# Kernel tuning notes

Measured on AMD Instinct MI355X. Metric: run time of the kernel, lower is better.

## Reference

```python
import jax, jax.numpy as jnp
import numpy as np

D_MODEL = 1024
N_HEADS = 16
MAX_SEQ_LEN = 2048

def setup_inputs() -> dict:
    key = jax.random.key(0)
    ks = jax.random.split(key, 4)
    B, L, D = 2, 2048, D_MODEL
    s = 0.02
    x = jax.random.normal(ks[0], (B, L, D), dtype=jnp.float32)
    qkv_w = jax.random.normal(ks[1], (D, 3 * D), dtype=jnp.float32) * s
    qkv_b = jnp.zeros((3 * D,), dtype=jnp.float32)
    proj_w = jax.random.normal(ks[2], (D, D), dtype=jnp.float32) * s
    proj_b = jnp.zeros((D,), dtype=jnp.float32)
    bias_table = jax.random.normal(ks[3], (2 * MAX_SEQ_LEN - 1, N_HEADS), dtype=jnp.float32) * s
    return {"x": x, "qkv_w": qkv_w, "qkv_b": qkv_b, "proj_w": proj_w, "proj_b": proj_b, "bias_table": bias_table}

def reference(x, qkv_w, qkv_b, proj_w, proj_b, bias_table):
    B, L, D = x.shape
    H = N_HEADS
    dk = D // H
    scale = dk ** -0.5
    # fused qkv projection: (B,L,3,H,dk)
    qkv = (x @ qkv_w + qkv_b).reshape(B, L, 3, H, dk)
    q = qkv[:, :, 0].transpose(0, 2, 1, 3)  # (B,H,L,dk)
    k = qkv[:, :, 1].transpose(0, 2, 1, 3)
    v = qkv[:, :, 2].transpose(0, 2, 1, 3)
    attn = jnp.einsum("bhqd,bhkd->bhqk", q, k) * scale  # (B,H,L,L)
    # relative position bias gather (Swin-style)
    coords = jnp.arange(L)
    rel_idx = coords[None, :] - coords[:, None] + (MAX_SEQ_LEN - 1)  # (L,L)
    rel_bias = bias_table[rel_idx]  # (L,L,H)
    attn = attn + rel_bias.transpose(2, 0, 1)[None]  # (B,H,L,L)
    attn = jax.nn.softmax(attn, axis=-1)
    out = jnp.einsum("bhqk,bhkd->bhqd", attn, v)  # (B,H,L,dk)
    out = out.transpose(0, 2, 1, 3).reshape(B, L, D)
    return out @ proj_w + proj_b
```

## Files before the change

kernel.cpp:

```cpp
#include <hip/hip_runtime.h>
#include <stdint.h>

typedef __attribute__((ext_vector_type(4))) float    f32x4;
typedef __attribute__((ext_vector_type(8))) short    bf16x8;
typedef __attribute__((ext_vector_type(2))) uint32_t u32x2;

#define MFMA16(a,b,c) __builtin_amdgcn_mfma_f32_16x16x32_bf16((a),(b),(c),0,0,0)

__device__ __forceinline__ uint16_t f2bf(float f){
  uint32_t u = __float_as_uint(f);
  return (uint16_t)((u + 0x7FFFu + ((u >> 16) & 1u)) >> 16);
}

__device__ __forceinline__ uint32_t pk_bf16(float lo, float hi){
  uint32_t r; asm("v_cvt_pk_bf16_f32 %0, %1, %2" : "=v"(r) : "v"(lo), "v"(hi)); return r;
}

__device__ __forceinline__ float fast_exp2(float x){
  float r; asm("v_exp_f32 %0, %1" : "=v"(r) : "v"(x)); return r;
}

__device__ __forceinline__ void gload16(const uint16_t* g, uint16_t* l){
  __builtin_amdgcn_global_load_lds((const __attribute__((address_space(1))) uint32_t*)g,
                                   (__attribute__((address_space(3))) uint32_t*)l, 16, 0, 0);
}

__global__ void k_cvt(const float* __restrict__ in, uint16_t* __restrict__ out){
  const size_t i = (size_t)(blockIdx.x*256 + threadIdx.x) * 4;
  const f32x4 v = *(const f32x4*)(in + i);
  u32x2 pk = {pk_bf16(v[0], v[1]), pk_bf16(v[2], v[3])};
  *(u32x2*)(out + i) = pk;
}

__global__ void k_tcvt(const float* __restrict__ in, uint16_t* __restrict__ out, int K, int N){
  __shared__ float tile[64][65];
  const int k0 = blockIdx.y*64, n0 = blockIdx.x*64;
  const int tc = threadIdx.x & 63, tr = threadIdx.x >> 6;
  #pragma unroll
  for (int p=0;p<16;p++){ int r = p*4 + tr; tile[r][tc] = in[(size_t)(k0+r)*N + n0 + tc]; }
  __syncthreads();
  #pragma unroll
  for (int p=0;p<16;p++){ int r = p*4 + tr; out[(size_t)(n0+r)*K + k0 + tc] = f2bf(tile[tc][r]); }
}

__global__ void k_biast(const float* __restrict__ in, float* __restrict__ out){
  const int i = blockIdx.x*256 + threadIdx.x;
  if (i < 4095*16) out[(i & 15)*4096 + (i >> 4)] = in[i] * 1.4426950408889634f;
}

template<int EPI>
__global__ __launch_bounds__(256, 2) void k_gemm(
    const uint16_t* __restrict__ A, const uint16_t* __restrict__ Bt,
    const float* __restrict__ bias,
    uint16_t* __restrict__ qo, uint16_t* __restrict__ ko, uint16_t* __restrict__ vto,
    float* __restrict__ outf)
{
  __shared__ __align__(16) uint16_t at[128*64];
  __shared__ __align__(16) uint16_t bt[128*64];
  const int tid = threadIdx.x;
  const int lane = tid & 63, w = tid >> 6;
  const int g = lane >> 4, li = lane & 15;
  const int wr = w >> 1, wc = w & 1;
  const int m0 = blockIdx.y * 128, n0 = blockIdx.x * 128;

  f32x4 acc[4][4] = {};

  const int srow = tid >> 3;
  const int scg  = (tid & 7) ^ (srow & 7);

  for (int kt_ = 0; kt_ < 16; kt_++){
    const int kk = kt_*64;
    __syncthreads();
    #pragma unroll
    for (int j = 0; j < 4; j++){
      gload16(A  + (size_t)(m0 + j*32 + srow)*1024 + kk + scg*8, at + (j*256+tid)*8);
      gload16(Bt + (size_t)(n0 + j*32 + srow)*1024 + kk + scg*8, bt + (j*256+tid)*8);
    }
    asm volatile("s_waitcnt vmcnt(0)" ::: "memory");
    __syncthreads();

    bf16x8 af[2][4], bfr[2][4];
    #pragma unroll
    for (int mi=0; mi<4; mi++){
      int row = wr*64 + mi*16 + li, sw = row & 7;
      af[0][mi] = *(const bf16x8*)(at + row*64 + ((g     ^ sw)*8));
      af[1][mi] = *(const bf16x8*)(at + row*64 + (((4+g) ^ sw)*8));
    }
    #pragma unroll
    for (int ni=0; ni<4; ni++){
      int row = wc*64 + ni*16 + li, sw = row & 7;
      bfr[0][ni] = *(const bf16x8*)(bt + row*64 + ((g     ^ sw)*8));
      bfr[1][ni] = *(const bf16x8*)(bt + row*64 + (((4+g) ^ sw)*8));
    }
    #pragma unroll
    for (int s=0; s<2; s++)
      #pragma unroll
      for (int mi=0; mi<4; mi++)
        #pragma unroll
        for (int ni=0; ni<4; ni++)
          acc[mi][ni] = MFMA16(af[s][mi], bfr[s][ni], acc[mi][ni]);
  }

  if (EPI == 0){
    #pragma unroll
    for (int ni=0; ni<4; ni++){
      const int c = n0 + wc*64 + ni*16 + li;
      const float bv = bias[c];
      const int which = c >> 10, cc = c & 1023;
      const int h = cc >> 6, d = cc & 63;
      #pragma unroll
      for (int mi=0; mi<4; mi++){
        const int trow = m0 + wr*64 + mi*16 + g*4;
        const int b_ = trow >> 11, lcl = trow & 2047;
        const f32x4 v4 = acc[mi][ni];
        if (which == 0){
          uint16_t* dst = qo + (((size_t)(b_*16 + h)*2048 + lcl)*64 + d);
          #pragma unroll
          for (int r=0;r<4;r++) dst[(size_t)r*64] = f2bf((v4[r] + bv) * 0.18033688011112042f);
        } else if (which == 1){
          uint16_t* dst = ko + (((size_t)(b_*16 + h)*2048 + lcl)*64 + d);
          #pragma unroll
          for (int r=0;r<4;r++) dst[(size_t)r*64] = f2bf(v4[r] + bv);
        } else {
          u32x2 pk = {pk_bf16(v4[0]+bv, v4[1]+bv), pk_bf16(v4[2]+bv, v4[3]+bv)};
          *(u32x2*)(vto + (((size_t)(b_*16 + h)*64 + d)*2048 + lcl)) = pk;
        }
      }
    }
  } else {
    #pragma unroll
    for (int ni=0; ni<4; ni++){
      const int c = n0 + wc*64 + ni*16 + li;
      const float bv = bias[c];
      #pragma unroll
      for (int mi=0; mi<4; mi++){
        const int trow = m0 + wr*64 + mi*16 + g*4;
        float* dst = outf + (size_t)trow*1024 + c;
        const f32x4 v4 = acc[mi][ni];
        #pragma unroll
        for (int r=0;r<4;r++) dst[(size_t)r*1024] = v4[r] + bv;
      }
    }
  }
}

__global__ __launch_bounds__(512, 4) void k_attn(
    const uint16_t* __restrict__ qg, const uint16_t* __restrict__ kg,
    const uint16_t* __restrict__ vg, const float* __restrict__ biast,
    uint16_t* __restrict__ outp)
{
  __shared__ __align__(16) uint16_t kt[2][64*64];
  __shared__ __align__(16) uint16_t vt[2][64*64];
  __shared__ __align__(16) uint16_t pt[8][16*64];
  __shared__ float bl[2176];
  const int tid = threadIdx.x;
  const int lane = tid & 63, w = tid >> 6;
  const int g = lane >> 4, li = lane & 15;
  const int bh = blockIdx.y, h = bh & 15, b_ = bh >> 4;
  const int qb0 = blockIdx.x * 128;

  for (int i = tid; i < 2175; i += 512) bl[i] = biast[h*4096 + 1920 - qb0 + i];

  bf16x8 qf[2];
  {
    const uint16_t* qp = qg + ((size_t)bh*2048 + qb0 + w*16 + li)*64 + g*8;
    qf[0] = *(const bf16x8*)(qp);
    qf[1] = *(const bf16x8*)(qp + 32);
  }
  f32x4 o[4] = {};
  float mrun = -__builtin_inff(), lrun = 0.f;
  const uint16_t* kbase = kg + (size_t)bh*(2048*64);
  const uint16_t* vbase = vg + (size_t)bh*(64*2048);
  const int srow = tid >> 3;
  const int scg  = (tid & 7) ^ (srow & 7);
  const int q_l = w*16 + li;
  uint16_t* pl = &pt[w][0];
  const int swp = li & 7;

  __syncthreads();

  gload16(kbase + (size_t)srow*64        + scg*8, &kt[0][tid*8]);
  gload16(vbase + (size_t)srow*2048      + scg*8, &vt[0][tid*8]);

  for (int t = 0; t < 32; t++){
    const int cur = t & 1;
    if (t < 31){
      const int kv1 = (t+1)*64;
      gload16(kbase + (size_t)(kv1 + srow)*64  + scg*8, &kt[cur^1][tid*8]);
      gload16(vbase + (size_t)srow*2048 + kv1  + scg*8, &vt[cur^1][tid*8]);
      asm volatile("s_waitcnt vmcnt(2)" ::: "memory");
    } else {
      asm volatile("s_waitcnt vmcnt(0)" ::: "memory");
    }
    __builtin_amdgcn_s_barrier();
    const uint16_t* ktc = &kt[cur][0];
    const uint16_t* vtc = &vt[cur][0];
    const int kv0 = t*64;

    f32x4 sa[4];
    #pragma unroll
    for (int mf=0; mf<4; mf++){
      const int row = mf*16 + li, sw = row & 7;
      bf16x8 a0 = *(const bf16x8*)(ktc + row*64 + ((g     ^ sw)*8));
      bf16x8 a1 = *(const bf16x8*)(ktc + row*64 + (((4+g) ^ sw)*8));
      f32x4 cfr = {};
      cfr = MFMA16(a0, qf[0], cfr);
      cfr = MFMA16(a1, qf[1], cfr);
      sa[mf] = cfr;
    }

    const int ib0 = kv0 + g*4 + 127 - q_l;
    float tmax = -__builtin_inff();
    #pragma unroll
    for (int mf=0; mf<4; mf++){
      #pragma unroll
      for (int r=0; r<4; r++){
        float vv = sa[mf][r] + bl[ib0 + mf*16 + r];
        sa[mf][r] = vv;
        tmax = fmaxf(tmax, vv);
      }
    }
    tmax = fmaxf(tmax, __shfl_xor(tmax, 16));
    tmax = fmaxf(tmax, __shfl_xor(tmax, 32));
    const float mnew = fmaxf(mrun, tmax);
    const float alpha = fast_exp2(mrun - mnew);
    mrun = mnew;
    lrun *= alpha;
    #pragma unroll
    for (int i=0;i<4;i++) o[i] *= alpha;
    float psum = 0.f;
    #pragma unroll
    for (int mf=0; mf<4; mf++){
      float p0 = fast_exp2(sa[mf][0] - mnew);
      float p1 = fast_exp2(sa[mf][1] - mnew);
      float p2 = fast_exp2(sa[mf][2] - mnew);
      float p3 = fast_exp2(sa[mf][3] - mnew);
      psum += (p0+p1)+(p2+p3);
      const int ch = (2*mf + (g>>1)) ^ swp;
      u32x2 pk = {pk_bf16(p0,p1), pk_bf16(p2,p3)};
      *(u32x2*)(pl + li*64 + ch*8 + (g&1)*4) = pk;
    }
    psum += __shfl_xor(psum, 16);
    psum += __shfl_xor(psum, 32);
    lrun += psum;

    #pragma unroll
    for (int s=0; s<2; s++){
      bf16x8 pb = *(const bf16x8*)(pl + li*64 + (((4*s+g) ^ swp)*8));
      #pragma unroll
      for (int mf=0; mf<4; mf++){
        const int row = mf*16 + li, sw = row & 7;
        bf16x8 av = *(const bf16x8*)(vtc + row*64 + (((4*s+g) ^ sw)*8));
        o[mf] = MFMA16(av, pb, o[mf]);
      }
    }
    __builtin_amdgcn_s_barrier();
  }

  const float inv = 1.0f / lrun;
  const size_t token = (size_t)b_*2048 + qb0 + w*16 + li;
  #pragma unroll
  for (int mf=0; mf<4; mf++){
    u32x2 pk = {pk_bf16(o[mf][0]*inv, o[mf][1]*inv), pk_bf16(o[mf][2]*inv, o[mf][3]*inv)};
    *(u32x2*)(outp + token*1024 + h*64 + mf*16 + g*4) = pk;
  }
}

extern "C" void kernel_launch(void* const* d_in, const int* in_sizes, int n_in,
                              void* d_out, int out_size, void* d_ws, size_t ws_size,
                              hipStream_t stream)
{
  const float* x      = (const float*)d_in[0];
  const float* qkv_w  = (const float*)d_in[1];
  const float* qkv_b  = (const float*)d_in[2];
  const float* proj_w = (const float*)d_in[3];
  const float* proj_b = (const float*)d_in[4];
  const float* btab   = (const float*)d_in[5];
  float* out = (float*)d_out;

  char* p = (char*)d_ws;
  uint16_t* x_bf    = (uint16_t*)(p);
  uint16_t* qkv_wt  = (uint16_t*)(p + 8388608);
  uint16_t* proj_wt = (uint16_t*)(p + 14680064);
  uint16_t* q_buf   = (uint16_t*)(p + 16777216);
  uint16_t* k_buf   = (uint16_t*)(p + 25165824);
  uint16_t* vt_buf  = (uint16_t*)(p + 33554432);
  uint16_t* ao_buf  = (uint16_t*)(p + 41943040);
  float*    bias_t  = (float*)   (p + 50331648);

  k_cvt  <<<dim3(4096),  dim3(256), 0, stream>>>(x, x_bf);
  k_tcvt <<<dim3(48,16), dim3(256), 0, stream>>>(qkv_w,  qkv_wt,  1024, 3072);
  k_tcvt <<<dim3(16,16), dim3(256), 0, stream>>>(proj_w, proj_wt, 1024, 1024);
  k_biast<<<dim3(256),   dim3(256), 0, stream>>>(btab, bias_t);

  k_gemm<0><<<dim3(24,32), dim3(256), 0, stream>>>(x_bf, qkv_wt, qkv_b, q_buf, k_buf, vt_buf, nullptr);
  k_attn   <<<dim3(16,32), dim3(512), 0, stream>>>(q_buf, k_buf, vt_buf, bias_t, ao_buf);
  k_gemm<1><<<dim3(8,32),  dim3(256), 0, stream>>>(ao_buf, proj_wt, proj_b, nullptr, nullptr, nullptr, out);
}
```

Measured before the change: 137.5 us.

## Restructure attention: 32 queries per wave, lazy rescale, MFMA row sums

The attention kernel now runs 256 threads per block, with each wave handling two 16-query chunks, so every K/V fragment read from LDS feeds twice as many MFMAs. The row-sum reduction is replaced by an extra MFMA against a ones vector. Max rescaling is skipped when the new max is within a threshold of the running max. Bias values are prefetched from global memory into registers one tile ahead instead of being staged through shared memory. This cuts LDS traffic, shuffles and exp work per tile, but raises register pressure and lowers wave count per block.

```diff
diff --git a/kernel.cpp b/kernel.cpp
--- a/kernel.cpp
+++ b/kernel.cpp
@@ -144,125 +144,180 @@
   }
 }
 
-__global__ __launch_bounds__(512, 4) void k_attn(
+__device__ __forceinline__ void attn_tile(
+    int t, bool last, int tid, int g, int li, int srow, int scg,
+    const uint16_t* kbase, const uint16_t* vbase, const float* bb,
+    const uint16_t* ktc, uint16_t* ktn, const uint16_t* vtc, uint16_t* vtn, uint16_t* pl,
+    const bf16x8 (&qf)[2][2], bf16x8 ones,
+    f32x4 (&o)[4][2], f32x4 (&o4)[2], float& mrun0, float& mrun1,
+    const float (&bvC)[2][4][4], float (&bvN)[2][4][4])
+{
+  if (!last){
+    const int kv1 = (t+1)*64;
+    gload16(kbase + (size_t)(kv1+srow)*64 + scg*8,         ktn + tid*8);
+    gload16(kbase + (size_t)(kv1+srow+32)*64 + scg*8,      ktn + 2048 + tid*8);
+    gload16(vbase + (size_t)srow*2048 + kv1 + scg*8,       vtn + tid*8);
+    gload16(vbase + (size_t)(srow+32)*2048 + kv1 + scg*8,  vtn + 2048 + tid*8);
+    #pragma unroll
+    for (int c=0;c<2;c++)
+      #pragma unroll
+      for (int mf=0;mf<4;mf++)
+        #pragma unroll
+        for (int r=0;r<4;r++)
+          bvN[c][mf][r] = bb[kv1 + mf*16 + g*4 + r - c*16 - li];
+    asm volatile("s_waitcnt vmcnt(36)" ::: "memory");
+  } else {
+    asm volatile("s_waitcnt vmcnt(0)" ::: "memory");
+  }
+  __builtin_amdgcn_s_barrier();
+
+  f32x4 sa[4][2];
+  #pragma unroll
+  for (int mf=0; mf<4; mf++){
+    const int row = mf*16 + li, sw = row & 7;
+    bf16x8 a0 = *(const bf16x8*)(ktc + row*64 + ((g     ^ sw)*8));
+    bf16x8 a1 = *(const bf16x8*)(ktc + row*64 + (((4+g) ^ sw)*8));
+    #pragma unroll
+    for (int c=0;c<2;c++){
+      f32x4 cfr = {};
+      cfr = MFMA16(a0, qf[c][0], cfr);
+      cfr = MFMA16(a1, qf[c][1], cfr);
+      sa[mf][c] = cfr;
+    }
+  }
+
+  float t0 = -__builtin_inff(), t1 = -__builtin_inff();
+  #pragma unroll
+  for (int mf=0; mf<4; mf++){
+    #pragma unroll
+    for (int r=0; r<4; r++){
+      sa[mf][0][r] += bvC[0][mf][r];
+      sa[mf][1][r] += bvC[1][mf][r];
+    }
+    t0 = fmaxf(t0, fmaxf(fmaxf(sa[mf][0][0], sa[mf][0][1]), fmaxf(sa[mf][0][2], sa[mf][0][3])));
+    t1 = fmaxf(t1, fmaxf(fmaxf(sa[mf][1][0], sa[mf][1][1]), fmaxf(sa[mf][1][2], sa[mf][1][3])));
+  }
+  t0 = fmaxf(t0, __shfl_xor(t0, 16)); t0 = fmaxf(t0, __shfl_xor(t0, 32));
+  t1 = fmaxf(t1, __shfl_xor(t1, 16)); t1 = fmaxf(t1, __shfl_xor(t1, 32));
+
+  const int ok = (t0 <= mrun0 + 8.f) && (t1 <= mrun1 + 8.f);
+  if (!__all(ok)){
+    const float mn0 = fmaxf(mrun0, t0), mn1 = fmaxf(mrun1, t1);
+    const float a0 = fast_exp2(mrun0 - mn0), a1 = fast_exp2(mrun1 - mn1);
+    #pragma unroll
+    for (int mf=0; mf<4; mf++){ o[mf][0] *= a0; o[mf][1] *= a1; }
+    o4[0] *= a0; o4[1] *= a1;
+    mrun0 = mn0; mrun1 = mn1;
+  }
+
+  const int swp2 = 2*(li & 7);
+  #pragma unroll
+  for (int c=0;c<2;c++){
+    const float mr = c ? mrun1 : mrun0;
+    #pragma unroll
+    for (int mf=0; mf<4; mf++){
+      float p0 = fast_exp2(sa[mf][c][0] - mr);
+      float p1 = fast_exp2(sa[mf][c][1] - mr);
+      float p2 = fast_exp2(sa[mf][c][2] - mr);
+      float p3 = fast_exp2(sa[mf][c][3] - mr);
+      u32x2 pk = {pk_bf16(p0,p1), pk_bf16(p2,p3)};
+      *(u32x2*)(pl + (c*16+li)*64 + (((4*mf+g) ^ swp2)*4)) = pk;
+    }
+  }
+
+  bf16x8 av[2][4];
+  #pragma unroll
+  for (int s=0; s<2; s++)
+    #pragma unroll
+    for (int mf=0; mf<4; mf++){
+      const int row = mf*16 + li, sw = row & 7;
+      av[s][mf] = *(const bf16x8*)(vtc + row*64 + (((4*s+g) ^ sw)*8));
+    }
+  #pragma unroll
+  for (int c=0;c<2;c++){
+    #pragma unroll
+    for (int s=0; s<2; s++){
+      bf16x8 pb = *(const bf16x8*)(pl + (c*16+li)*64 + (((8*s+2*g) ^ swp2)*4));
+      o4[c] = MFMA16(ones, pb, o4[c]);
+      #pragma unroll
+      for (int mf=0; mf<4; mf++)
+        o[mf][c] = MFMA16(av[s][mf], pb, o[mf][c]);
+    }
+  }
+  __builtin_amdgcn_s_barrier();
+}
+
+__global__ __launch_bounds__(256, 2) void k_attn(
     const uint16_t* __restrict__ qg, const uint16_t* __restrict__ kg,
     const uint16_t* __restrict__ vg, const float* __restrict__ biast,
     uint16_t* __restrict__ outp)
 {
   __shared__ __align__(16) uint16_t kt[2][64*64];
   __shared__ __align__(16) uint16_t vt[2][64*64];
-  __shared__ __align__(16) uint16_t pt[8][16*64];
-  __shared__ float bl[2176];
+  __shared__ __align__(16) uint16_t pt[4][32*64];
   const int tid = threadIdx.x;
   const int lane = tid & 63, w = tid >> 6;
   const int g = lane >> 4, li = lane & 15;
   const int bh = blockIdx.y, h = bh & 15, b_ = bh >> 4;
   const int qb0 = blockIdx.x * 128;
-
-  for (int i = tid; i < 2175; i += 512) bl[i] = biast[h*4096 + 1920 - qb0 + i];
-
-  bf16x8 qf[2];
-  {
-    const uint16_t* qp = qg + ((size_t)bh*2048 + qb0 + w*16 + li)*64 + g*8;
-    qf[0] = *(const bf16x8*)(qp);
-    qf[1] = *(const bf16x8*)(qp + 32);
-  }
-  f32x4 o[4] = {};
-  float mrun = -__builtin_inff(), lrun = 0.f;
+  const int qw = qb0 + w*32;
+
+  bf16x8 qf[2][2];
+  #pragma unroll
+  for (int c=0;c<2;c++){
+    const uint16_t* qp = qg + ((size_t)bh*2048 + qw + c*16 + li)*64 + g*8;
+    qf[c][0] = *(const bf16x8*)(qp);
+    qf[c][1] = *(const bf16x8*)(qp + 32);
+  }
+  bf16x8 ones = (bf16x8)(short)0;
+  if (li == 0){ const short v = (short)0x3F80; ones = (bf16x8){v,v,v,v,v,v,v,v}; }
+
+  f32x4 o[4][2] = {};
+  f32x4 o4[2] = {};
+  float mrun0 = -__builtin_inff(), mrun1 = -__builtin_inff();
+
   const uint16_t* kbase = kg + (size_t)bh*(2048*64);
   const uint16_t* vbase = vg + (size_t)bh*(64*2048);
   const int srow = tid >> 3;
   const int scg  = (tid & 7) ^ (srow & 7);
-  const int q_l = w*16 + li;
+  const float* bb = biast + h*4096 + 2047 - qw;
   uint16_t* pl = &pt[w][0];
-  const int swp = li & 7;
-
-  __syncthreads();
-
-  gload16(kbase + (size_t)srow*64        + scg*8, &kt[0][tid*8]);
-  gload16(vbase + (size_t)srow*2048      + scg*8, &vt[0][tid*8]);
-
-  for (int t = 0; t < 32; t++){
-    const int cur = t & 1;
-    if (t < 31){
-      const int kv1 = (t+1)*64;
-      gload16(kbase + (size_t)(kv1 + srow)*64  + scg*8, &kt[cur^1][tid*8]);
-      gload16(vbase + (size_t)srow*2048 + kv1  + scg*8, &vt[cur^1][tid*8]);
-      asm volatile("s_waitcnt vmcnt(2)" ::: "memory");
-    } else {
-      asm volatile("s_waitcnt vmcnt(0)" ::: "memory");
-    }
-    __builtin_amdgcn_s_barrier();
-    const uint16_t* ktc = &kt[cur][0];
-    const uint16_t* vtc = &vt[cur][0];
-    const int kv0 = t*64;
-
-    f32x4 sa[4];
+
+  gload16(kbase + (size_t)srow*64 + scg*8,         &kt[0][tid*8]);
+  gload16(kbase + (size_t)(srow+32)*64 + scg*8,    &kt[0][2048 + tid*8]);
+  gload16(vbase + (size_t)srow*2048 + scg*8,       &vt[0][tid*8]);
+  gload16(vbase + (size_t)(srow+32)*2048 + scg*8,  &vt[0][2048 + tid*8]);
+  float bvA[2][4][4], bvB[2][4][4];
+  #pragma unroll
+  for (int c=0;c<2;c++)
+    #pragma unroll
+    for (int mf=0;mf<4;mf++)
+      #pragma unroll
+      for (int r=0;r<4;r++)
+        bvA[c][mf][r] = bb[mf*16 + g*4 + r - c*16 - li];
+
+  for (int tt = 0; tt < 32; tt += 2){
+    attn_tile(tt,   false,    tid, g, li, srow, scg, kbase, vbase, bb,
+              &kt[0][0], &kt[1][0], &vt[0][0], &vt[1][0], pl,
+              qf, ones, o, o4, mrun0, mrun1, bvA, bvB);
+    attn_tile(tt+1, tt == 30, tid, g, li, srow, scg, kbase, vbase, bb,
+              &kt[1][0], &kt[0][0], &vt[1][0], &vt[0][0], pl,
+              qf, ones, o, o4, mrun0, mrun1, bvB, bvA);
+  }
+
+  const float ls0 = __shfl(o4[0][0], li);
+  const float ls1 = __shfl(o4[1][0], li);
+  const float inv0 = 1.0f / ls0, inv1 = 1.0f / ls1;
+  #pragma unroll
+  for (int c=0;c<2;c++){
+    const float inv = c ? inv1 : inv0;
+    const size_t token = (size_t)b_*2048 + qw + c*16 + li;
     #pragma unroll
     for (int mf=0; mf<4; mf++){
-      const int row = mf*16 + li, sw = row & 7;
-      bf16x8 a0 = *(const bf16x8*)(ktc + row*64 + ((g     ^ sw)*8));
-      bf16x8 a1 = *(const bf16x8*)(ktc + row*64 + (((4+g) ^ sw)*8));
-      f32x4 cfr = {};
-      cfr = MFMA16(a0, qf[0], cfr);
-      cfr = MFMA16(a1, qf[1], cfr);
-      sa[mf] = cfr;
-    }
-
-    const int ib0 = kv0 + g*4 + 127 - q_l;
-    float tmax = -__builtin_inff();
-    #pragma unroll
-    for (int mf=0; mf<4; mf++){
-      #pragma unroll
-      for (int r=0; r<4; r++){
-        float vv = sa[mf][r] + bl[ib0 + mf*16 + r];
-        sa[mf][r] = vv;
-        tmax = fmaxf(tmax, vv);
-      }
-    }
-    tmax = fmaxf(tmax, __shfl_xor(tmax, 16));
-    tmax = fmaxf(tmax, __shfl_xor(tmax, 32));
-    const float mnew = fmaxf(mrun, tmax);
-    const float alpha = fast_exp2(mrun - mnew);
-    mrun = mnew;
-    lrun *= alpha;
-    #pragma unroll
-    for (int i=0;i<4;i++) o[i] *= alpha;
-    float psum = 0.f;
-    #pragma unroll
-    for (int mf=0; mf<4; mf++){
-      float p0 = fast_exp2(sa[mf][0] - mnew);
-      float p1 = fast_exp2(sa[mf][1] - mnew);
-      float p2 = fast_exp2(sa[mf][2] - mnew);
-      float p3 = fast_exp2(sa[mf][3] - mnew);
-      psum += (p0+p1)+(p2+p3);
-      const int ch = (2*mf + (g>>1)) ^ swp;
-      u32x2 pk = {pk_bf16(p0,p1), pk_bf16(p2,p3)};
-      *(u32x2*)(pl + li*64 + ch*8 + (g&1)*4) = pk;
-    }
-    psum += __shfl_xor(psum, 16);
-    psum += __shfl_xor(psum, 32);
-    lrun += psum;
-
-    #pragma unroll
-    for (int s=0; s<2; s++){
-      bf16x8 pb = *(const bf16x8*)(pl + li*64 + (((4*s+g) ^ swp)*8));
-      #pragma unroll
-      for (int mf=0; mf<4; mf++){
-        const int row = mf*16 + li, sw = row & 7;
-        bf16x8 av = *(const bf16x8*)(vtc + row*64 + (((4*s+g) ^ sw)*8));
-        o[mf] = MFMA16(av, pb, o[mf]);
-      }
-    }
-    __builtin_amdgcn_s_barrier();
-  }
-
-  const float inv = 1.0f / lrun;
-  const size_t token = (size_t)b_*2048 + qb0 + w*16 + li;
-  #pragma unroll
-  for (int mf=0; mf<4; mf++){
-    u32x2 pk = {pk_bf16(o[mf][0]*inv, o[mf][1]*inv), pk_bf16(o[mf][2]*inv, o[mf][3]*inv)};
-    *(u32x2*)(outp + token*1024 + h*64 + mf*16 + g*4) = pk;
+      u32x2 pk = {pk_bf16(o[mf][c][0]*inv, o[mf][c][1]*inv),
+                  pk_bf16(o[mf][c][2]*inv, o[mf][c][3]*inv)};
+      *(u32x2*)(outp + token*1024 + h*64 + mf*16 + g*4) = pk;
+    }
   }
 }
 
@@ -294,6 +349,6 @@
   k_biast<<<dim3(256),   dim3(256), 0, stream>>>(btab, bias_t);
 
   k_gemm<0><<<dim3(24,32), dim3(256), 0, stream>>>(x_bf, qkv_wt, qkv_b, q_buf, k_buf, vt_buf, nullptr);
-  k_attn   <<<dim3(16,32), dim3(512), 0, stream>>>(q_buf, k_buf, vt_buf, bias_t, ao_buf);
+  k_attn   <<<dim3(16,32), dim3(256), 0, stream>>>(q_buf, k_buf, vt_buf, bias_t, ao_buf);
   k_gemm<1><<<dim3(8,32),  dim3(256), 0, stream>>>(ao_buf, proj_wt, proj_b, nullptr, nullptr, nullptr, out);
 }
```

New measurement: 132.7 us. 1.04x faster.
